# Kernel optimization log

Hardware: AMD Instinct MI355X
Metric: run time of the kernel (lower is better)

Reference implementation:

```python
import jax, jax.numpy as jnp
import numpy as np

D_MODEL = 64
NUM_HEADS = 4
HEAD_DIM = D_MODEL // NUM_HEADS  # 16
SEQ_LEN = 8192


def setup_inputs() -> dict:
    key = jax.random.key(0)
    kx, kq, kk, kv, kbq, kbk, kbv = jax.random.split(key, 7)
    bound = 1.0 / np.sqrt(D_MODEL)  # torch nn.Linear default init range
    x = jax.random.normal(kx, (SEQ_LEN, D_MODEL), dtype=jnp.float32)
    Wq = jax.random.uniform(kq, (HEAD_DIM, D_MODEL), minval=-bound, maxval=bound, dtype=jnp.float32)
    Wk = jax.random.uniform(kk, (HEAD_DIM, D_MODEL), minval=-bound, maxval=bound, dtype=jnp.float32)
    Wv = jax.random.uniform(kv, (HEAD_DIM, D_MODEL), minval=-bound, maxval=bound, dtype=jnp.float32)
    bq = jax.random.uniform(kbq, (HEAD_DIM,), minval=-bound, maxval=bound, dtype=jnp.float32)
    bk = jax.random.uniform(kbk, (HEAD_DIM,), minval=-bound, maxval=bound, dtype=jnp.float32)
    bv = jax.random.uniform(kbv, (HEAD_DIM,), minval=-bound, maxval=bound, dtype=jnp.float32)
    return {"x": x, "Wq": Wq, "bq": bq, "Wk": Wk, "bk": bk, "Wv": Wv, "bv": bv}


def reference(x, Wq, bq, Wk, bk, Wv, bv):
    # Linear projections (torch nn.Linear: x @ W.T + b)
    Q = x @ Wq.T + bq  # [S, HEAD_DIM]
    K = x @ Wk.T + bk  # [S, HEAD_DIM]
    V = x @ Wv.T + bv  # [S, HEAD_DIM]
    scale = 1.0 / np.sqrt(HEAD_DIM).astype(np.float32)
    scores = (Q @ K.T) * scale  # [S, S]
    # causal mask: triu(ones, diagonal=1) positions set to -inf
    s = scores.shape[-1]
    causal = jnp.tril(jnp.ones((s, s), dtype=bool))  # True = keep
    scores = jnp.where(causal, scores, -jnp.inf)
    attn = jax.nn.softmax(scores, axis=-1)
    return attn @ V  # [S, HEAD_DIM]
```

## Files before the change

kernel.cpp:

```cpp
#include <hip/hip_runtime.h>
#include <hip/hip_fp16.h>

#define SEQ 8192
#define NQT 512
#define CHUNK 32
#define TOTAL_CHUNKS 4352

typedef _Float16 half4  __attribute__((ext_vector_type(4)));
typedef float   floatx4 __attribute__((ext_vector_type(4)));

__device__ __forceinline__ int cum_chunks(int n) {
    const int a = n >> 5, r = n & 31;
    return n + 16 * a * (a - 1) + a * r;
}

__global__ __launch_bounds__(256) void proj_kernel(
    const float* __restrict__ x,
    const float* __restrict__ Wq, const float* __restrict__ bq,
    const float* __restrict__ Wk, const float* __restrict__ bk,
    const float* __restrict__ Wv, const float* __restrict__ bv,
    _Float16* __restrict__ Q, _Float16* __restrict__ K, _Float16* __restrict__ VB)
{
    __shared__ float xs[16][65];
    __shared__ float wqs[16][65];
    __shared__ float wks[16][65];
    __shared__ float wvs[16][65];

    const int tid  = threadIdx.x;
    const int r    = tid >> 4;
    const int d    = tid & 15;
    const int row0 = blockIdx.x * 16;

    const int i4 = tid * 4;
    const int rr = i4 >> 6, cc = i4 & 63;
    {
        float4 v = *(const float4*)(x + (size_t)row0 * 64 + i4);
        xs[rr][cc] = v.x; xs[rr][cc+1] = v.y; xs[rr][cc+2] = v.z; xs[rr][cc+3] = v.w;
    }
    {
        float4 v = *(const float4*)(Wq + i4);
        wqs[rr][cc] = v.x; wqs[rr][cc+1] = v.y; wqs[rr][cc+2] = v.z; wqs[rr][cc+3] = v.w;
    }
    {
        float4 v = *(const float4*)(Wk + i4);
        wks[rr][cc] = v.x; wks[rr][cc+1] = v.y; wks[rr][cc+2] = v.z; wks[rr][cc+3] = v.w;
    }
    {
        float4 v = *(const float4*)(Wv + i4);
        wvs[rr][cc] = v.x; wvs[rr][cc+1] = v.y; wvs[rr][cc+2] = v.z; wvs[rr][cc+3] = v.w;
    }
    __syncthreads();

    float aq = 0.f, ak = 0.f, av = 0.f;
#pragma unroll
    for (int k = 0; k < 64; ++k) {
        float xv = xs[r][k];
        aq += xv * wqs[d][k];
        ak += xv * wks[d][k];
        av += xv * wvs[d][k];
    }
    aq += bq[d];
    ak += bk[d];
    av += bv[d];
    aq *= 0.36067376022224085f;

    const int row = row0 + r;
    Q[row * 16 + d] = (_Float16)aq;
    K[row * 16 + d] = (_Float16)ak;
    VB[(size_t)blockIdx.x * 256 + d * 16 + r] = (_Float16)av;
}

__global__ __launch_bounds__(64) void flash_kernel(
    const _Float16* __restrict__ Q, const _Float16* __restrict__ K,
    const _Float16* __restrict__ VB,
    float* __restrict__ partO, float* __restrict__ partL)
{
    const int bp = (TOTAL_CHUNKS - 1) - (int)blockIdx.x;
    int lo = 0, hi = NQT - 1;
#pragma unroll
    for (int it = 0; it < 9; ++it) {
        const int mid = (lo + hi + 1) >> 1;
        if (cum_chunks(mid) <= bp) lo = mid; else hi = mid - 1;
    }
    const int qt = lo;
    const int c  = bp - cum_chunks(qt);
    const int t0 = c * CHUNK;
    int t1 = t0 + CHUNK;
    if (t1 > qt + 1) t1 = qt + 1;
    const int nd = (t1 > qt) ? qt : t1;

    const int L    = threadIdx.x;
    const int m16  = L & 15;
    const int quad = L >> 4;
    const int qrow = qt * 16 + m16;

    const half4 qf = *(const half4*)(Q + (size_t)qrow * 16 + quad * 4);
    const _Float16* kbase = K  + (size_t)m16 * 16 + quad * 4;
    const _Float16* vbase = VB + (size_t)m16 * 16 + quad * 4;

    float   l0 = 0.f, l1 = 0.f;
    floatx4 acc0 = {0.f, 0.f, 0.f, 0.f};
    floatx4 acc1 = {0.f, 0.f, 0.f, 0.f};
    const floatx4 z4 = {0.f, 0.f, 0.f, 0.f};

    auto body = [&](half4 kf, half4 vf, floatx4& acc, float& ls) {
        floatx4 s = __builtin_amdgcn_mfma_f32_16x16x16f16(kf, qf, z4, 0, 0, 0);
        const float p0 = __builtin_amdgcn_exp2f(s[0]);
        const float p1 = __builtin_amdgcn_exp2f(s[1]);
        const float p2 = __builtin_amdgcn_exp2f(s[2]);
        const float p3 = __builtin_amdgcn_exp2f(s[3]);
        ls += (p0 + p1) + (p2 + p3);
        const half4 pf = {(_Float16)p0, (_Float16)p1, (_Float16)p2, (_Float16)p3};
        acc = __builtin_amdgcn_mfma_f32_16x16x16f16(vf, pf, acc, 0, 0, 0);
    };

    int kt = t0;
    if (kt + 1 < nd) {
        half4 kf0 = *(const half4*)(kbase + (size_t)kt * 256);
        half4 vf0 = *(const half4*)(vbase + (size_t)kt * 256);
        half4 kf1 = *(const half4*)(kbase + (size_t)(kt + 1) * 256);
        half4 vf1 = *(const half4*)(vbase + (size_t)(kt + 1) * 256);
#pragma unroll 2
        for (; kt + 3 < nd; kt += 2) {
            const half4 nk0 = *(const half4*)(kbase + (size_t)(kt + 2) * 256);
            const half4 nv0 = *(const half4*)(vbase + (size_t)(kt + 2) * 256);
            const half4 nk1 = *(const half4*)(kbase + (size_t)(kt + 3) * 256);
            const half4 nv1 = *(const half4*)(vbase + (size_t)(kt + 3) * 256);
            body(kf0, vf0, acc0, l0);
            body(kf1, vf1, acc1, l1);
            kf0 = nk0; vf0 = nv0; kf1 = nk1; vf1 = nv1;
        }
        body(kf0, vf0, acc0, l0);
        body(kf1, vf1, acc1, l1);
        kt += 2;
    }
    for (; kt < nd; ++kt)
        body(*(const half4*)(kbase + (size_t)kt * 256),
             *(const half4*)(vbase + (size_t)kt * 256), acc0, l0);

    if (t1 == qt + 1) {
        const int k0 = qt * 16;
        const half4 kf = *(const half4*)(kbase + (size_t)qt * 256);
        floatx4 s = __builtin_amdgcn_mfma_f32_16x16x16f16(kf, qf, z4, 0, 0, 0);
#pragma unroll
        for (int r = 0; r < 4; ++r)
            if (k0 + quad * 4 + r > qrow) s[r] = -1.0e30f;
        const float p0 = __builtin_amdgcn_exp2f(s[0]);
        const float p1 = __builtin_amdgcn_exp2f(s[1]);
        const float p2 = __builtin_amdgcn_exp2f(s[2]);
        const float p3 = __builtin_amdgcn_exp2f(s[3]);
        l1 += (p0 + p1) + (p2 + p3);
        const half4 pf = {(_Float16)p0, (_Float16)p1, (_Float16)p2, (_Float16)p3};
        const half4 vf = *(const half4*)(vbase + (size_t)qt * 256);
        acc1 = __builtin_amdgcn_mfma_f32_16x16x16f16(vf, pf, acc1, 0, 0, 0);
    }

    floatx4 acc = {acc0[0] + acc1[0], acc0[1] + acc1[1],
                   acc0[2] + acc1[2], acc0[3] + acc1[3]};
    float lsum = l0 + l1;
    lsum += __shfl_xor(lsum, 16);
    lsum += __shfl_xor(lsum, 32);

    *(floatx4*)(partO + (size_t)bp * 256 + m16 * 16 + quad * 4) = acc;
    if (quad == 0) partL[(size_t)bp * 16 + m16] = lsum;
}

__global__ __launch_bounds__(256) void merge_kernel(
    const float* __restrict__ partO, const float* __restrict__ partL,
    float* __restrict__ out)
{
    const int qt = blockIdx.x;
    const int t  = threadIdx.x;

    const int base = cum_chunks(qt);
    const int nc   = (qt >> 5) + 1;

    const float* po = partO + (size_t)base * 256 + t;
    const float* pl = partL + (size_t)base * 16 + (t >> 4);
    float Ls = 0.f, O = 0.f;
    for (int c = 0; c < nc; ++c, po += 256, pl += 16) {
        O  += *po;
        Ls += *pl;
    }
    out[(size_t)qt * 256 + t] = O / Ls;
}

extern "C" void kernel_launch(void* const* d_in, const int* in_sizes, int n_in,
                              void* d_out, int out_size, void* d_ws, size_t ws_size,
                              hipStream_t stream) {
    const float* x  = (const float*)d_in[0];
    const float* Wq = (const float*)d_in[1];
    const float* bq = (const float*)d_in[2];
    const float* Wk = (const float*)d_in[3];
    const float* bk = (const float*)d_in[4];
    const float* Wv = (const float*)d_in[5];
    const float* bv = (const float*)d_in[6];

    char* ws = (char*)d_ws;
    _Float16* Q     = (_Float16*)(ws);
    _Float16* K     = (_Float16*)(ws + 262144);
    _Float16* VB    = (_Float16*)(ws + 524288);
    float*    partO = (float*)(ws + 786432);
    float*    partL = (float*)(ws + 786432 + 4456448);

    proj_kernel<<<dim3(SEQ / 16), dim3(256), 0, stream>>>(
        x, Wq, bq, Wk, bk, Wv, bv, Q, K, VB);
    flash_kernel<<<dim3(TOTAL_CHUNKS), dim3(64), 0, stream>>>(
        Q, K, VB, partO, partL);
    merge_kernel<<<dim3(NQT), dim3(256), 0, stream>>>(
        partO, partL, (float*)d_out);
}
```

Measured before the change: 87.03 us.

## Interleave K and V per lane into one half8 load, vectorize projection LDS

The projection kernel now writes K and V into one interleaved buffer. Each flash-kernel lane can then fetch its K fragment and V fragment with a single 16-byte load instead of two 8-byte loads, which halves the number of global load instructions in the hot loop. The projection kernel also stores and reads shared memory as float4 rows, and the flash loop raises wave priority around the MFMA/exp block with s_setprio. The risks are the more complex layout indexing and possible changes in how the scheduler treats the priority hint.

```diff
diff --git a/kernel.cpp b/kernel.cpp
--- a/kernel.cpp
+++ b/kernel.cpp
@@ -7,6 +7,7 @@
 #define TOTAL_CHUNKS 4352
 
 typedef _Float16 half4  __attribute__((ext_vector_type(4)));
+typedef _Float16 half8  __attribute__((ext_vector_type(8)));
 typedef float   floatx4 __attribute__((ext_vector_type(4)));
 
 __device__ __forceinline__ int cum_chunks(int n) {
@@ -19,45 +20,36 @@
     const float* __restrict__ Wq, const float* __restrict__ bq,
     const float* __restrict__ Wk, const float* __restrict__ bk,
     const float* __restrict__ Wv, const float* __restrict__ bv,
-    _Float16* __restrict__ Q, _Float16* __restrict__ K, _Float16* __restrict__ VB)
+    _Float16* __restrict__ Q, _Float16* __restrict__ KV)
 {
-    __shared__ float xs[16][65];
-    __shared__ float wqs[16][65];
-    __shared__ float wks[16][65];
-    __shared__ float wvs[16][65];
+    __shared__ float4 xs[16][17];
+    __shared__ float4 wqs[16][17];
+    __shared__ float4 wks[16][17];
+    __shared__ float4 wvs[16][17];
 
     const int tid  = threadIdx.x;
     const int r    = tid >> 4;
     const int d    = tid & 15;
     const int row0 = blockIdx.x * 16;
 
-    const int i4 = tid * 4;
-    const int rr = i4 >> 6, cc = i4 & 63;
-    {
-        float4 v = *(const float4*)(x + (size_t)row0 * 64 + i4);
-        xs[rr][cc] = v.x; xs[rr][cc+1] = v.y; xs[rr][cc+2] = v.z; xs[rr][cc+3] = v.w;
-    }
-    {
-        float4 v = *(const float4*)(Wq + i4);
-        wqs[rr][cc] = v.x; wqs[rr][cc+1] = v.y; wqs[rr][cc+2] = v.z; wqs[rr][cc+3] = v.w;
-    }
-    {
-        float4 v = *(const float4*)(Wk + i4);
-        wks[rr][cc] = v.x; wks[rr][cc+1] = v.y; wks[rr][cc+2] = v.z; wks[rr][cc+3] = v.w;
-    }
-    {
-        float4 v = *(const float4*)(Wv + i4);
-        wvs[rr][cc] = v.x; wvs[rr][cc+1] = v.y; wvs[rr][cc+2] = v.z; wvs[rr][cc+3] = v.w;
-    }
+    const int rr  = tid >> 4;
+    const int cc4 = tid & 15;
+    xs[rr][cc4]  = *(const float4*)(x  + (size_t)row0 * 64 + tid * 4);
+    wqs[rr][cc4] = *(const float4*)(Wq + tid * 4);
+    wks[rr][cc4] = *(const float4*)(Wk + tid * 4);
+    wvs[rr][cc4] = *(const float4*)(Wv + tid * 4);
     __syncthreads();
 
     float aq = 0.f, ak = 0.f, av = 0.f;
 #pragma unroll
-    for (int k = 0; k < 64; ++k) {
-        float xv = xs[r][k];
-        aq += xv * wqs[d][k];
-        ak += xv * wks[d][k];
-        av += xv * wvs[d][k];
+    for (int kk = 0; kk < 16; ++kk) {
+        const float4 xv = xs[r][kk];
+        const float4 q4 = wqs[d][kk];
+        const float4 k4 = wks[d][kk];
+        const float4 v4 = wvs[d][kk];
+        aq += xv.x * q4.x; aq += xv.y * q4.y; aq += xv.z * q4.z; aq += xv.w * q4.w;
+        ak += xv.x * k4.x; ak += xv.y * k4.y; ak += xv.z * k4.z; ak += xv.w * k4.w;
+        av += xv.x * v4.x; av += xv.y * v4.y; av += xv.z * v4.z; av += xv.w * v4.w;
     }
     aq += bq[d];
     ak += bk[d];
@@ -66,13 +58,13 @@
 
     const int row = row0 + r;
     Q[row * 16 + d] = (_Float16)aq;
-    K[row * 16 + d] = (_Float16)ak;
-    VB[(size_t)blockIdx.x * 256 + d * 16 + r] = (_Float16)av;
+    _Float16* kvb = KV + (size_t)blockIdx.x * 512;
+    kvb[((d >> 2) * 16 + r) * 8 + (d & 3)]     = (_Float16)ak;
+    kvb[((r >> 2) * 16 + d) * 8 + 4 + (r & 3)] = (_Float16)av;
 }
 
 __global__ __launch_bounds__(64) void flash_kernel(
-    const _Float16* __restrict__ Q, const _Float16* __restrict__ K,
-    const _Float16* __restrict__ VB,
+    const _Float16* __restrict__ Q, const _Float16* __restrict__ KV,
     float* __restrict__ partO, float* __restrict__ partL)
 {
     const int bp = (TOTAL_CHUNKS - 1) - (int)blockIdx.x;
@@ -95,15 +87,20 @@
     const int qrow = qt * 16 + m16;
 
     const half4 qf = *(const half4*)(Q + (size_t)qrow * 16 + quad * 4);
-    const _Float16* kbase = K  + (size_t)m16 * 16 + quad * 4;
-    const _Float16* vbase = VB + (size_t)m16 * 16 + quad * 4;
+    const _Float16* kvbase = KV + (size_t)L * 8;
 
     float   l0 = 0.f, l1 = 0.f;
     floatx4 acc0 = {0.f, 0.f, 0.f, 0.f};
     floatx4 acc1 = {0.f, 0.f, 0.f, 0.f};
     const floatx4 z4 = {0.f, 0.f, 0.f, 0.f};
 
-    auto body = [&](half4 kf, half4 vf, floatx4& acc, float& ls) {
+    auto ldkv = [&](int t) -> half8 {
+        return *(const half8*)(kvbase + (size_t)t * 512);
+    };
+
+    auto body = [&](half8 kv, floatx4& acc, float& ls) {
+        const half4 kf = __builtin_shufflevector(kv, kv, 0, 1, 2, 3);
+        const half4 vf = __builtin_shufflevector(kv, kv, 4, 5, 6, 7);
         floatx4 s = __builtin_amdgcn_mfma_f32_16x16x16f16(kf, qf, z4, 0, 0, 0);
         const float p0 = __builtin_amdgcn_exp2f(s[0]);
         const float p1 = __builtin_amdgcn_exp2f(s[1]);
@@ -116,31 +113,30 @@
 
     int kt = t0;
     if (kt + 1 < nd) {
-        half4 kf0 = *(const half4*)(kbase + (size_t)kt * 256);
-        half4 vf0 = *(const half4*)(vbase + (size_t)kt * 256);
-        half4 kf1 = *(const half4*)(kbase + (size_t)(kt + 1) * 256);
-        half4 vf1 = *(const half4*)(vbase + (size_t)(kt + 1) * 256);
+        half8 kv0 = ldkv(kt);
+        half8 kv1 = ldkv(kt + 1);
 #pragma unroll 2
         for (; kt + 3 < nd; kt += 2) {
-            const half4 nk0 = *(const half4*)(kbase + (size_t)(kt + 2) * 256);
-            const half4 nv0 = *(const half4*)(vbase + (size_t)(kt + 2) * 256);
-            const half4 nk1 = *(const half4*)(kbase + (size_t)(kt + 3) * 256);
-            const half4 nv1 = *(const half4*)(vbase + (size_t)(kt + 3) * 256);
-            body(kf0, vf0, acc0, l0);
-            body(kf1, vf1, acc1, l1);
-            kf0 = nk0; vf0 = nv0; kf1 = nk1; vf1 = nv1;
+            const half8 n0 = ldkv(kt + 2);
+            const half8 n1 = ldkv(kt + 3);
+            __builtin_amdgcn_s_setprio(1);
+            body(kv0, acc0, l0);
+            body(kv1, acc1, l1);
+            __builtin_amdgcn_s_setprio(0);
+            kv0 = n0; kv1 = n1;
         }
-        body(kf0, vf0, acc0, l0);
-        body(kf1, vf1, acc1, l1);
+        body(kv0, acc0, l0);
+        body(kv1, acc1, l1);
         kt += 2;
     }
     for (; kt < nd; ++kt)
-        body(*(const half4*)(kbase + (size_t)kt * 256),
-             *(const half4*)(vbase + (size_t)kt * 256), acc0, l0);
+        body(ldkv(kt), acc0, l0);
 
     if (t1 == qt + 1) {
         const int k0 = qt * 16;
-        const half4 kf = *(const half4*)(kbase + (size_t)qt * 256);
+        const half8 kv = ldkv(qt);
+        const half4 kf = __builtin_shufflevector(kv, kv, 0, 1, 2, 3);
+        const half4 vf = __builtin_shufflevector(kv, kv, 4, 5, 6, 7);
         floatx4 s = __builtin_amdgcn_mfma_f32_16x16x16f16(kf, qf, z4, 0, 0, 0);
 #pragma unroll
         for (int r = 0; r < 4; ++r)
@@ -151,7 +147,6 @@
         const float p3 = __builtin_amdgcn_exp2f(s[3]);
         l1 += (p0 + p1) + (p2 + p3);
         const half4 pf = {(_Float16)p0, (_Float16)p1, (_Float16)p2, (_Float16)p3};
-        const half4 vf = *(const half4*)(vbase + (size_t)qt * 256);
         acc1 = __builtin_amdgcn_mfma_f32_16x16x16f16(vf, pf, acc1, 0, 0, 0);
     }
 
@@ -198,15 +193,14 @@
 
     char* ws = (char*)d_ws;
     _Float16* Q     = (_Float16*)(ws);
-    _Float16* K     = (_Float16*)(ws + 262144);
-    _Float16* VB    = (_Float16*)(ws + 524288);
+    _Float16* KV    = (_Float16*)(ws + 262144);
     float*    partO = (float*)(ws + 786432);
     float*    partL = (float*)(ws + 786432 + 4456448);
 
     proj_kernel<<<dim3(SEQ / 16), dim3(256), 0, stream>>>(
-        x, Wq, bq, Wk, bk, Wv, bv, Q, K, VB);
+        x, Wq, bq, Wk, bk, Wv, bv, Q, KV);
     flash_kernel<<<dim3(TOTAL_CHUNKS), dim3(64), 0, stream>>>(
-        Q, K, VB, partO, partL);
+        Q, KV, partO, partL);
     merge_kernel<<<dim3(NQT), dim3(256), 0, stream>>>(
         partO, partL, (float*)d_out);
 }
```

New measurement: 83.99 us. -3.5%, faster.
